# Kernel optimization log

Hardware: AMD Instinct MI355X
Metric: run time of the kernel (lower is better)

## Reference

```python
import jax, jax.numpy as jnp
import numpy as np

N = 100000   # nodes
E = 1600000  # edges (avg degree 16)
IN, H, OUT = 128, 128, 64
EPS = 1e-5


def setup_inputs() -> dict:
    key = jax.random.key(0)
    ks = jax.random.split(key, 8)

    def glorot(k, i, o):
        s = 1.0 / np.sqrt(i)
        return jax.random.uniform(k, (i, o), jnp.float32, -s, s)

    return {
        "x": jax.random.normal(ks[0], (N, IN), jnp.float32),
        "edge_index": jax.random.randint(ks[1], (2, E), 0, N, dtype=jnp.int32),
        "W1": glorot(ks[2], IN, H), "b1": jnp.zeros((H,), jnp.float32),
        "g1": jnp.ones((H,), jnp.float32), "be1": jnp.zeros((H,), jnp.float32),
        "W2": glorot(ks[3], H, H), "b2": jnp.zeros((H,), jnp.float32),
        "g2": jnp.ones((H,), jnp.float32), "be2": jnp.zeros((H,), jnp.float32),
        "W3": glorot(ks[4], H, OUT), "b3": jnp.zeros((OUT,), jnp.float32),
    }


def gcn_conv(x, W, b, src, dst):
    # PyG GCNConv: add self-loops, symmetric norm D^-1/2 (A+I) D^-1/2, then x@W, bias after aggregation.
    n = x.shape[0]
    h = x @ W                                   # [N, out]
    deg = jnp.zeros((n,), h.dtype).at[dst].add(1.0) + 1.0  # +1 for self-loop
    dis = jax.lax.rsqrt(deg)                    # deg^-1/2
    coef = dis[src] * dis[dst]                  # per-edge norm
    agg = jnp.zeros_like(h).at[dst].add(h[src] * coef[:, None])
    agg = agg + h * (dis * dis)[:, None]        # self-loop messages
    return agg + b


def batch_norm(x, g, b):
    # BatchNorm1d in training mode: batch statistics over nodes, biased variance.
    m = x.mean(axis=0)
    v = x.var(axis=0)
    return (x - m) * jax.lax.rsqrt(v + EPS) * g + b


def reference(x, edge_index, W1, b1, g1, be1, W2, b2, g2, be2, W3, b3):
    src, dst = edge_index[0], edge_index[1]
    h = gcn_conv(x, W1, b1, src, dst)
    h = batch_norm(h, g1, be1)
    h = gcn_conv(h, W2, b2, src, dst)
    h = batch_norm(h, g2, be2)
    out = gcn_conv(h, W3, b3, src, dst)
    return out
```

## Files before the change

### kernel.cpp

```cpp
#include <hip/hip_runtime.h>
#include <hip/hip_fp16.h>


constexpr int BSH = 7;
constexpr int NXCD = 8;

typedef _Float16 half8 __attribute__((ext_vector_type(8)));
typedef float f32x4 __attribute__((ext_vector_type(4)));

static __device__ inline ushort f2h(float f) {
    union { __half h; ushort u; } cv;
    cv.h = __float2half_rn(f);
    return cv.u;
}
static __device__ inline float2 h2f2(unsigned int u) {
    union { unsigned int u; __half2 h; } cv;
    cv.u = u;
    return __half22float2(cv.h);
}
static __device__ inline __half2 u2h2(unsigned int u) {
    union { unsigned int u; __half2 h; } cv;
    cv.u = u;
    return cv.h;
}

#define ACCPK(v) do { \
    acch[0] = __hadd2(acch[0], u2h2((v).x)); \
    acch[1] = __hadd2(acch[1], u2h2((v).y)); \
    acch[2] = __hadd2(acch[2], u2h2((v).z)); \
    acch[3] = __hadd2(acch[3], u2h2((v).w)); \
} while (0)

__global__ __launch_bounds__(256) void countwt_k(const int* __restrict__ dst,
                                                 int* __restrict__ hist,
                                                 int E, int EPB, int nbuk,
                                                 const float* __restrict__ W1,
                                                 const float* __restrict__ W2,
                                                 const float* __restrict__ W3,
                                                 ushort* __restrict__ wt1,
                                                 ushort* __restrict__ wt2,
                                                 ushort* __restrict__ wt3) {
    if (blockIdx.x < 3) {
        const float* W; ushort* WT; int OUTD;
        if (blockIdx.x == 0)      { W = W1; WT = wt1; OUTD = 128; }
        else if (blockIdx.x == 1) { W = W2; WT = wt2; OUTD = 128; }
        else                      { W = W3; WT = wt3; OUTD = 64; }
        const int tot = 128 * OUTD;
        for (int idx = threadIdx.x; idx < tot; idx += 256) {
            int nq = idx >> 7;
            int k  = idx & 127;
            WT[idx] = f2h(W[k * OUTD + nq]);
        }
        return;
    }
    const int bid = blockIdx.x - 3;
    __shared__ int lh[1024];
    for (int i = threadIdx.x; i < nbuk; i += 256) lh[i] = 0;
    __syncthreads();
    const int e0 = bid * EPB;
    const int e1 = min(e0 + EPB, E);
    for (int e = e0 + threadIdx.x; e < e1; e += 256)
        atomicAdd(&lh[dst[e] >> BSH], 1);
    __syncthreads();
    const int xcd = bid & (NXCD - 1);
    for (int i = threadIdx.x; i < nbuk; i += 256) {
        int v = lh[i];
        if (v) atomicAdd(&hist[xcd * nbuk + i], v);
    }
}

__global__ __launch_bounds__(256) void scan_hist_k(const int* __restrict__ hist,
                                                   int* __restrict__ cur,
                                                   int* __restrict__ bstart,
                                                   int* __restrict__ row_ptr,
                                                   float* __restrict__ stats,
                                                   int nbuk, int n, int E) {
    stats[threadIdx.x] = 0.f;
    stats[threadIdx.x + 256] = 0.f;
    const int NT = nbuk * NXCD;
    const int C = (NT + 255) / 256;
    int vals[32];
    const int tid = threadIdx.x;
    int sum = 0;
#pragma unroll
    for (int k = 0; k < 32; ++k) {
        if (k >= C) break;
        int key = tid * C + k;
        int v = 0;
        if (key < NT) {
            int b = key >> 3, x = key & 7;
            v = hist[x * nbuk + b];
        }
        vals[k] = v;
        sum += v;
    }
    __shared__ int part[256];
    part[tid] = sum;
    __syncthreads();
    for (int off = 1; off < 256; off <<= 1) {
        int t = 0;
        if (tid >= off) t = part[tid - off];
        __syncthreads();
        part[tid] += t;
        __syncthreads();
    }
    int run = (tid == 0) ? 0 : part[tid - 1];
#pragma unroll
    for (int k = 0; k < 32; ++k) {
        if (k >= C) break;
        int key = tid * C + k;
        if (key < NT) {
            int b = key >> 3, x = key & 7;
            cur[x * nbuk + b] = run;
            if (x == 0) bstart[b] = run;
        }
        run += vals[k];
    }
    if (tid == 0) { bstart[nbuk] = E; row_ptr[n] = E; }
}

__global__ __launch_bounds__(256) void scatter_bucket_k(const int* __restrict__ src,
                                                        const int* __restrict__ dst,
                                                        int* __restrict__ cur,
                                                        unsigned int* __restrict__ ebuf,
                                                        int E, int EPB, int nbuk) {
    __shared__ int lh[1024];
    __shared__ int base[1024];
    for (int i = threadIdx.x; i < nbuk; i += 256) lh[i] = 0;
    __syncthreads();
    const int e0 = blockIdx.x * EPB;
    const int e1 = min(e0 + EPB, E);
    const int xcd = blockIdx.x & (NXCD - 1);
    for (int e = e0 + threadIdx.x; e < e1; e += 256)
        atomicAdd(&lh[dst[e] >> BSH], 1);
    __syncthreads();
    for (int i = threadIdx.x; i < nbuk; i += 256) {
        int v = lh[i];
        base[i] = v ? atomicAdd(&cur[xcd * nbuk + i], v) : 0;
        lh[i] = 0;
    }
    __syncthreads();
    for (int e = e0 + threadIdx.x; e < e1; e += 256) {
        int d = dst[e];
        int s = src[e];
        int b = d >> BSH;
        int pos = base[b] + atomicAdd(&lh[b], 1);
        ebuf[pos] = ((unsigned int)s << BSH) | (unsigned int)(d & 127);
    }
}

__global__ __launch_bounds__(256) void bucket_sort_k(const unsigned int* __restrict__ ebuf,
                                                     const int* __restrict__ bstart,
                                                     int* __restrict__ row_ptr,
                                                     int* __restrict__ esrc,
                                                     float* __restrict__ dis, int n) {
    const int b = blockIdx.x;
    const int beg = bstart[b];
    const int end = bstart[b + 1];
    __shared__ int cnt[128], off[128];
    if (threadIdx.x < 128) cnt[threadIdx.x] = 0;
    __syncthreads();
    for (int i = beg + threadIdx.x; i < end; i += 256)
        atomicAdd(&cnt[ebuf[i] & 127], 1);
    __syncthreads();
    if (threadIdx.x < 128) off[threadIdx.x] = cnt[threadIdx.x];
    __syncthreads();
    for (int d = 1; d < 128; d <<= 1) {
        int t = 0;
        if (threadIdx.x < 128 && threadIdx.x >= d) t = off[threadIdx.x - d];
        __syncthreads();
        if (threadIdx.x < 128) off[threadIdx.x] += t;
        __syncthreads();
    }
    if (threadIdx.x < 128) {
        int deg = cnt[threadIdx.x];
        int ex = off[threadIdx.x] - deg;
        int node = (b << BSH) + threadIdx.x;
        if (node < n) {
            row_ptr[node] = beg + ex;
            dis[node] = rsqrtf((float)deg + 1.0f);
        }
        cnt[threadIdx.x] = ex;
    }
    __syncthreads();
    for (int i = beg + threadIdx.x; i < end; i += 256) {
        unsigned int p = ebuf[i];
        int l = (int)(p & 127);
        int pos = beg + atomicAdd(&cnt[l], 1);
        esrc[pos] = (int)(p >> BSH);
    }
}

template <int OUTD, bool XF16, bool BNIN>
__global__ __launch_bounds__(256) void gemm_reg_k(const void* __restrict__ Xv,
                                                  const ushort* __restrict__ WT,
                                                  const float* __restrict__ sums,
                                                  const float* __restrict__ gg,
                                                  const float* __restrict__ be,
                                                  const float* __restrict__ dis,
                                                  ushort* __restrict__ Hs, int nn) {
    constexpr int NCT = OUTD / 16;
    __shared__ __align__(16) float s_scale[BNIN ? 128 : 4];
    __shared__ __align__(16) float s_shift[BNIN ? 128 : 4];
    if (BNIN) {
        if (threadIdx.x < 128) {
            int c = threadIdx.x;
            float inv_n = 1.0f / (float)nn;
            float m = sums[c] * inv_n;
            float v = sums[c + 128] * inv_n - m * m;
            float sc = rsqrtf(v + 1e-5f) * gg[c];
            s_scale[c] = sc;
            s_shift[c] = be[c] - m * sc;
        }
        __syncthreads();
    }

    const int wave = threadIdx.x >> 6;
    const int lane = threadIdx.x & 63;
    const int l15 = lane & 15;
    const int kg = lane >> 4;
    const int row = blockIdx.x * 64 + wave * 16 + l15;

    half8 a[4];
#pragma unroll
    for (int kk = 0; kk < 4; ++kk) {
        float v[8];
        if (row < nn) {
            if (XF16) {
                const uint4* xp = (const uint4*)((const ushort*)Xv + (size_t)row * 128
                                                 + kk * 32 + kg * 8);
                uint4 raw = *xp;
                float2 f;
                f = h2f2(raw.x); v[0] = f.x; v[1] = f.y;
                f = h2f2(raw.y); v[2] = f.x; v[3] = f.y;
                f = h2f2(raw.z); v[4] = f.x; v[5] = f.y;
                f = h2f2(raw.w); v[6] = f.x; v[7] = f.y;
            } else {
                const float4* xp = (const float4*)((const float*)Xv + (size_t)row * 128
                                                   + kk * 32 + kg * 8);
                float4 v0 = xp[0];
                float4 v1 = xp[1];
                v[0] = v0.x; v[1] = v0.y; v[2] = v0.z; v[3] = v0.w;
                v[4] = v1.x; v[5] = v1.y; v[6] = v1.z; v[7] = v1.w;
            }
            if (BNIN) {
                int kq = kk * 8 + kg * 2;
                float4 s0 = ((const float4*)s_scale)[kq];
                float4 s1 = ((const float4*)s_scale)[kq + 1];
                float4 h0 = ((const float4*)s_shift)[kq];
                float4 h1 = ((const float4*)s_shift)[kq + 1];
                v[0] = v[0] * s0.x + h0.x;
                v[1] = v[1] * s0.y + h0.y;
                v[2] = v[2] * s0.z + h0.z;
                v[3] = v[3] * s0.w + h0.w;
                v[4] = v[4] * s1.x + h1.x;
                v[5] = v[5] * s1.y + h1.y;
                v[6] = v[6] * s1.z + h1.z;
                v[7] = v[7] * s1.w + h1.w;
            }
#pragma unroll
            for (int j = 0; j < 8; ++j) a[kk][j] = (_Float16)v[j];
        } else {
#pragma unroll
            for (int j = 0; j < 8; ++j) a[kk][j] = (_Float16)0.f;
        }
    }

    f32x4 acc[NCT];
#pragma unroll
    for (int ct = 0; ct < NCT; ++ct) acc[ct] = (f32x4){0.f, 0.f, 0.f, 0.f};

#pragma unroll
    for (int kk = 0; kk < 4; ++kk) {
#pragma unroll
        for (int ct = 0; ct < NCT; ++ct) {
            half8 bfr = *(const half8*)&WT[(ct * 16 + l15) * 128 + kk * 32 + kg * 8];
            acc[ct] = __builtin_amdgcn_mfma_f32_16x16x32_f16(a[kk], bfr, acc[ct], 0, 0, 0);
        }
    }

    const int mbase = blockIdx.x * 64 + wave * 16 + kg * 4;
    float dm[4];
#pragma unroll
    for (int reg = 0; reg < 4; ++reg) {
        int m = mbase + reg;
        dm[reg] = (m < nn) ? dis[m] : 0.f;
    }
#pragma unroll
    for (int ct = 0; ct < NCT; ++ct) {
        int ncol = ct * 16 + l15;
        size_t cb = (size_t)(ncol >> 5) * nn * 32 + (ncol & 31);
#pragma unroll
        for (int reg = 0; reg < 4; ++reg) {
            int m = mbase + reg;
            if (m < nn) Hs[cb + (size_t)m * 32] = f2h(acc[ct][reg] * dm[reg]);
        }
    }
}

template <int OUTD, bool STATS, bool OUTF16>
__global__ __launch_bounds__(256) void gather_k(const ushort* __restrict__ Hs,
                                                const float* __restrict__ dis,
                                                const float* __restrict__ b,
                                                const int* __restrict__ row_ptr,
                                                const int* __restrict__ esrc,
                                                void* __restrict__ Ov,
                                                float* __restrict__ sums,
                                                float* __restrict__ sumsq, int n) {
    constexpr int NCHUNK = OUTD / 32;

    __shared__ float s_sum[32];
    __shared__ float s_sq[32];
    if (STATS) {
        if (threadIdx.x < 32) { s_sum[threadIdx.x] = 0.f; s_sq[threadIdx.x] = 0.f; }
        __syncthreads();
    }

    const int chunk = blockIdx.x & (NCHUNK - 1);
    const int nblk  = blockIdx.x / NCHUNK;
    const int g     = threadIdx.x >> 2;
    const int lane  = threadIdx.x & 3;
    const int node  = nblk * 64 + g;

    __half2 acch[4];
#pragma unroll
    for (int c = 0; c < 4; ++c) acch[c] = __half2(__float2half_rn(0.f), __float2half_rn(0.f));
    float o[8];
#pragma unroll
    for (int c = 0; c < 8; ++c) o[c] = 0.f;

    if (node < n) {
        const uint4* Hc = (const uint4*)Hs + (size_t)chunk * n * 4;

        {
            uint4 v = Hc[(size_t)node * 4 + lane];
            ACCPK(v);
        }
        const int beg = row_ptr[node];
        const int end = row_ptr[node + 1];
        int j = beg;
        const int end8 = beg + ((end - beg) & ~7);
        for (; j < end8; j += 8) {
            int s[8];
#pragma unroll
            for (int u = 0; u < 8; ++u) s[u] = esrc[j + u];
            uint4 va[8];
#pragma unroll
            for (int u = 0; u < 8; ++u) va[u] = Hc[(size_t)s[u] * 4 + lane];
#pragma unroll
            for (int u = 0; u < 8; ++u) { ACCPK(va[u]); }
        }
        for (; j < end; ++j) {
            int s = esrc[j];
            uint4 a = Hc[(size_t)s * 4 + lane];
            ACCPK(a);
        }

        float dd = dis[node];
        const float4* B4 = (const float4*)b + chunk * 8 + lane * 2;
        float4 b0 = B4[0];
        float4 b1 = B4[1];
        float2 f0 = __half22float2(acch[0]);
        float2 f1 = __half22float2(acch[1]);
        float2 f2 = __half22float2(acch[2]);
        float2 f3 = __half22float2(acch[3]);
        o[0] = f0.x * dd + b0.x;
        o[1] = f0.y * dd + b0.y;
        o[2] = f1.x * dd + b0.z;
        o[3] = f1.y * dd + b0.w;
        o[4] = f2.x * dd + b1.x;
        o[5] = f2.y * dd + b1.y;
        o[6] = f3.x * dd + b1.z;
        o[7] = f3.y * dd + b1.w;

        if (OUTF16) {
            union { ushort us[8]; uint4 v; } pk;
#pragma unroll
            for (int c = 0; c < 8; ++c) pk.us[c] = f2h(o[c]);
            ((uint4*)Ov)[(size_t)node * (OUTD / 8) + chunk * 4 + lane] = pk.v;
        } else {
            float4* O4 = (float4*)Ov + (size_t)node * (OUTD / 4) + chunk * 8 + lane * 2;
            O4[0] = make_float4(o[0], o[1], o[2], o[3]);
            O4[1] = make_float4(o[4], o[5], o[6], o[7]);
        }
    }

    if (STATS) {
        float sv[8], qv[8];
#pragma unroll
        for (int c = 0; c < 8; ++c) { sv[c] = o[c]; qv[c] = o[c] * o[c]; }
#pragma unroll
        for (int c = 0; c < 8; ++c) {
#pragma unroll
            for (int m = 4; m <= 32; m <<= 1) {
                sv[c] += __shfl_xor(sv[c], m);
                qv[c] += __shfl_xor(qv[c], m);
            }
        }
        if ((threadIdx.x & 63) < 4) {
            int c0 = lane * 8;
#pragma unroll
            for (int c = 0; c < 8; ++c) {
                atomicAdd(&s_sum[c0 + c], sv[c]);
                atomicAdd(&s_sq[c0 + c], qv[c]);
            }
        }
        __syncthreads();
        if (threadIdx.x < 32) {
            atomicAdd(&sums[chunk * 32 + threadIdx.x], s_sum[threadIdx.x]);
            atomicAdd(&sumsq[chunk * 32 + threadIdx.x], s_sq[threadIdx.x]);
        }
    }
}

extern "C" void kernel_launch(void* const* d_in, const int* in_sizes, int n_in,
                              void* d_out, int out_size, void* d_ws, size_t ws_size,
                              hipStream_t stream) {
    const float* x   = (const float*)d_in[0];
    const int*   ei  = (const int*)d_in[1];
    const float* W1  = (const float*)d_in[2];
    const float* b1  = (const float*)d_in[3];
    const float* g1  = (const float*)d_in[4];
    const float* be1 = (const float*)d_in[5];
    const float* W2  = (const float*)d_in[6];
    const float* b2  = (const float*)d_in[7];
    const float* g2  = (const float*)d_in[8];
    const float* be2 = (const float*)d_in[9];
    const float* W3  = (const float*)d_in[10];
    const float* b3  = (const float*)d_in[11];
    float* out = (float*)d_out;

    const int N = in_sizes[0] / 128;
    const int E = in_sizes[1] / 2;
    const int* src = ei;
    const int* dst = ei + E;
    const int NBUK = (N + 127) >> BSH;

    float* wsp   = (float*)d_ws;
    float* dis   = wsp;
    float* stats = wsp + N;
    ushort* wt1  = (ushort*)(stats + 512);
    ushort* wt2  = wt1 + 128 * 128;
    ushort* wt3  = wt2 + 128 * 128;
    int*   hist   = (int*)(wt3 + 128 * 64);
    int*   cur    = hist + NBUK * NXCD;
    int*   bstart = cur + NBUK * NXCD;
    int*   row_ptr = bstart + NBUK + 1 + 63;
    float* bufA  = (float*)((((uintptr_t)(row_ptr + N + 1)) + 255) & ~(uintptr_t)255);
    float* bufB  = bufA + (size_t)N * 128;
    unsigned int* ebuf = (unsigned int*)(bufB + (size_t)N * 128);
    int*   esrc  = (int*)(ebuf + E);

    ushort* Hs  = (ushort*)bufA;
    ushort* Bf16 = (ushort*)bufB;

    float* statsA = stats;
    float* statsB = stats + 256;

    const int BS = 256;
    dim3 blk(BS);
    const int SGRID = 128;
    const int EPB = (E + SGRID - 1) / SGRID;

    hipMemsetAsync(hist, 0, (size_t)NBUK * NXCD * 4, stream);
    countwt_k<<<dim3(SGRID + 3), blk, 0, stream>>>(dst, hist, E, EPB, NBUK,
                                                   W1, W2, W3, wt1, wt2, wt3);
    scan_hist_k<<<dim3(1), blk, 0, stream>>>(hist, cur, bstart, row_ptr, stats, NBUK, N, E);
    scatter_bucket_k<<<dim3(SGRID), blk, 0, stream>>>(src, dst, cur, ebuf, E, EPB, NBUK);
    bucket_sort_k<<<dim3(NBUK), blk, 0, stream>>>(ebuf, bstart, row_ptr, esrc, dis, N);

    const int gemm_grid = (N + 63) / 64;
    const int NBg = (N + 63) / 64;

    gemm_reg_k<128, false, false><<<dim3(gemm_grid), blk, 0, stream>>>(
        x, wt1, nullptr, nullptr, nullptr, dis, Hs, N);
    gather_k<128, true, true><<<dim3(NBg * 4), blk, 0, stream>>>(
        Hs, dis, b1, row_ptr, esrc, Bf16, statsA, statsA + 128, N);

    gemm_reg_k<128, true, true><<<dim3(gemm_grid), blk, 0, stream>>>(
        Bf16, wt2, statsA, g1, be1, dis, Hs, N);
    gather_k<128, true, true><<<dim3(NBg * 4), blk, 0, stream>>>(
        Hs, dis, b2, row_ptr, esrc, Bf16, statsB, statsB + 128, N);

    gemm_reg_k<64, true, true><<<dim3(gemm_grid), blk, 0, stream>>>(
        Bf16, wt3, statsB, g2, be2, dis, Hs, N);
    gather_k<64, false, false><<<dim3(NBg * 2), blk, 0, stream>>>(
        Hs, dis, b3, row_ptr, esrc, out, nullptr, nullptr, N);
}
```

Before: 404.7 us.

## Sort nodes by degree within buckets to balance gather wavefront work

The bucket sort kernel now runs a shared-memory bitonic sort of each 128-node bucket by in-degree and writes a node permutation. The gather kernels map each 4-thread group to perm[i] instead of i, so nodes sharing a wavefront have similar neighbor counts. This is meant to cut idle lanes in the edge loops caused by uneven degrees. The cost is an extra bitonic sort with many syncs per bucket, one extra indirection load per node, and slightly less contiguous output writes.

```diff
diff --git a/kernel.cpp b/kernel.cpp
--- a/kernel.cpp
+++ b/kernel.cpp
@@ -153,11 +153,13 @@
                                                      const int* __restrict__ bstart,
                                                      int* __restrict__ row_ptr,
                                                      int* __restrict__ esrc,
-                                                     float* __restrict__ dis, int n) {
+                                                     float* __restrict__ dis,
+                                                     int* __restrict__ perm, int n) {
     const int b = blockIdx.x;
     const int beg = bstart[b];
     const int end = bstart[b + 1];
     __shared__ int cnt[128], off[128];
+    __shared__ unsigned int dkey[128];
     if (threadIdx.x < 128) cnt[threadIdx.x] = 0;
     __syncthreads();
     for (int i = beg + threadIdx.x; i < end; i += 256)
@@ -176,10 +178,13 @@
         int deg = cnt[threadIdx.x];
         int ex = off[threadIdx.x] - deg;
         int node = (b << BSH) + threadIdx.x;
+        unsigned int dv = 0xFFFFFFu;
         if (node < n) {
             row_ptr[node] = beg + ex;
             dis[node] = rsqrtf((float)deg + 1.0f);
-        }
+            dv = (unsigned int)deg;
+        }
+        dkey[threadIdx.x] = (dv << 7) | (unsigned int)threadIdx.x;
         cnt[threadIdx.x] = ex;
     }
     __syncthreads();
@@ -189,6 +194,22 @@
         int pos = beg + atomicAdd(&cnt[l], 1);
         esrc[pos] = (int)(p >> BSH);
     }
+    for (int k = 2; k <= 128; k <<= 1) {
+        for (int j = k >> 1; j > 0; j >>= 1) {
+            __syncthreads();
+            if (threadIdx.x < 64) {
+                int i = threadIdx.x;
+                int xi = ((i & ~(j - 1)) << 1) | (i & (j - 1));
+                int yi = xi | j;
+                unsigned int a = dkey[xi], c = dkey[yi];
+                bool asc = (xi & k) == 0;
+                if ((a > c) == asc) { dkey[xi] = c; dkey[yi] = a; }
+            }
+        }
+    }
+    __syncthreads();
+    if (threadIdx.x < 128)
+        perm[(b << BSH) + threadIdx.x] = (b << BSH) + (int)(dkey[threadIdx.x] & 127u);
 }
 
 template <int OUTD, bool XF16, bool BNIN>
@@ -304,6 +325,7 @@
                                                 const float* __restrict__ b,
                                                 const int* __restrict__ row_ptr,
                                                 const int* __restrict__ esrc,
+                                                const int* __restrict__ perm,
                                                 void* __restrict__ Ov,
                                                 float* __restrict__ sums,
                                                 float* __restrict__ sumsq, int n) {
@@ -320,7 +342,7 @@
     const int nblk  = blockIdx.x / NCHUNK;
     const int g     = threadIdx.x >> 2;
     const int lane  = threadIdx.x & 3;
-    const int node  = nblk * 64 + g;
+    const int node  = perm[nblk * 64 + g];
 
     __half2 acch[4];
 #pragma unroll
@@ -450,6 +472,7 @@
     float* bufB  = bufA + (size_t)N * 128;
     unsigned int* ebuf = (unsigned int*)(bufB + (size_t)N * 128);
     int*   esrc  = (int*)(ebuf + E);
+    int*   perm  = esrc + E;
 
     ushort* Hs  = (ushort*)bufA;
     ushort* Bf16 = (ushort*)bufB;
@@ -467,7 +490,7 @@
                                                    W1, W2, W3, wt1, wt2, wt3);
     scan_hist_k<<<dim3(1), blk, 0, stream>>>(hist, cur, bstart, row_ptr, stats, NBUK, N, E);
     scatter_bucket_k<<<dim3(SGRID), blk, 0, stream>>>(src, dst, cur, ebuf, E, EPB, NBUK);
-    bucket_sort_k<<<dim3(NBUK), blk, 0, stream>>>(ebuf, bstart, row_ptr, esrc, dis, N);
+    bucket_sort_k<<<dim3(NBUK), blk, 0, stream>>>(ebuf, bstart, row_ptr, esrc, dis, perm, N);
 
     const int gemm_grid = (N + 63) / 64;
     const int NBg = (N + 63) / 64;
@@ -475,15 +498,15 @@
     gemm_reg_k<128, false, false><<<dim3(gemm_grid), blk, 0, stream>>>(
         x, wt1, nullptr, nullptr, nullptr, dis, Hs, N);
     gather_k<128, true, true><<<dim3(NBg * 4), blk, 0, stream>>>(
-        Hs, dis, b1, row_ptr, esrc, Bf16, statsA, statsA + 128, N);
+        Hs, dis, b1, row_ptr, esrc, perm, Bf16, statsA, statsA + 128, N);
 
     gemm_reg_k<128, true, true><<<dim3(gemm_grid), blk, 0, stream>>>(
         Bf16, wt2, statsA, g1, be1, dis, Hs, N);
     gather_k<128, true, true><<<dim3(NBg * 4), blk, 0, stream>>>(
-        Hs, dis, b2, row_ptr, esrc, Bf16, statsB, statsB + 128, N);
+        Hs, dis, b2, row_ptr, esrc, perm, Bf16, statsB, statsB + 128, N);
 
     gemm_reg_k<64, true, true><<<dim3(gemm_grid), blk, 0, stream>>>(
         Bf16, wt3, statsB, g2, be2, dis, Hs, N);
     gather_k<64, false, false><<<dim3(NBg * 2), blk, 0, stream>>>(
-        Hs, dis, b3, row_ptr, esrc, out, nullptr, nullptr, N);
-}
+        Hs, dis, b3, row_ptr, esrc, perm, out, nullptr, nullptr, N);
+}
```

New measurement: 429.0 us. +6.0%, slower.
